# Kernel optimization log

Measured on AMD Instinct MI355X. Metric: run time of the kernel, lower is better.

## Reference

```python
import jax, jax.numpy as jnp
import numpy as np

N_NODES = 50000
N_EDGES = 800000
N_GRAPHS = 256
HEADS = 4
HID = 64
HC = HEADS * HID  # 256
EMB = 256
RADIUS = 3
EPS_BN = 1e-5
NEG_SLOPE = 0.2  # PyG GATConv default


def _init(key, shape, fan_in):
    return jax.random.normal(key, shape, jnp.float32) / np.sqrt(fan_in).astype(np.float32)


def setup_inputs() -> dict:
    key = jax.random.key(0)
    ks = jax.random.split(key, 12)
    x = jax.random.normal(ks[0], (N_NODES, 9), jnp.float32)
    edge_index = jax.random.randint(ks[1], (2, N_EDGES), 0, N_NODES)
    batch = jnp.sort(jax.random.randint(ks[2], (N_NODES,), 0, N_GRAPHS))
    W0 = _init(ks[3], (9, HC), 9)
    att_src0 = _init(ks[4], (HEADS, HID), HID)
    att_dst0 = _init(ks[5], (HEADS, HID), HID)
    bias0 = jnp.zeros((HC,), jnp.float32)
    W12 = _init(ks[6], (2, HC, HC), HC)
    att_src12 = _init(ks[7], (2, HEADS, HID), HID)
    att_dst12 = _init(ks[8], (2, HEADS, HID), HID)
    bias12 = jnp.zeros((2, HC), jnp.float32)
    gamma = jnp.ones((RADIUS, HC), jnp.float32)
    beta = jnp.zeros((RADIUS, HC), jnp.float32)
    Wm1 = _init(ks[9], (HC, EMB), HC)
    bm1 = jnp.zeros((EMB,), jnp.float32)
    Wm2 = _init(ks[10], (EMB, EMB), EMB)
    bm2 = jnp.zeros((EMB,), jnp.float32)
    return dict(x=x, edge_index=edge_index, batch=batch, W0=W0, att_src0=att_src0,
                att_dst0=att_dst0, bias0=bias0, W12=W12, att_src12=att_src12,
                att_dst12=att_dst12, bias12=bias12, gamma=gamma, beta=beta,
                Wm1=Wm1, bm1=bm1, Wm2=Wm2, bm2=bm2)


def gat_conv(x, src, dst, W, a_src, a_dst, bias):
    # PyG GATConv (concat=True), self-loops already appended to src/dst.
    N = x.shape[0]
    h = (x @ W).reshape(N, HEADS, HID)                 # [N,H,C]
    al_src = jnp.einsum('nhc,hc->nh', h, a_src)        # [N,H]
    al_dst = jnp.einsum('nhc,hc->nh', h, a_dst)
    e = jax.nn.leaky_relu(al_src[src] + al_dst[dst], NEG_SLOPE)  # [E,H]
    # segment softmax over incoming edges of each dst node
    e_max = jax.ops.segment_max(e, dst, num_segments=N)
    e = jnp.exp(e - e_max[dst])
    denom = jax.ops.segment_sum(e, dst, num_segments=N)
    alpha = e / (denom[dst] + 1e-16)                   # [E,H]
    msg = alpha[:, :, None] * h[src]                   # [E,H,C]
    out = jax.ops.segment_sum(msg, dst, num_segments=N)  # [N,H,C]
    return out.reshape(N, HC) + bias


def batch_norm(x, g, b):
    mu = x.mean(axis=0)
    var = x.var(axis=0)
    return (x - mu) * jax.lax.rsqrt(var + EPS_BN) * g + b


def reference(x, edge_index, batch, W0, att_src0, att_dst0, bias0, W12, att_src12,
              att_dst12, bias12, gamma, beta, Wm1, bm1, Wm2, bm2):
    loops = jnp.arange(N_NODES, dtype=edge_index.dtype)
    src = jnp.concatenate([edge_index[0], loops])
    dst = jnp.concatenate([edge_index[1], loops])
    Ws = [W0, W12[0], W12[1]]
    a_s = [att_src0, att_src12[0], att_src12[1]]
    a_d = [att_dst0, att_dst12[0], att_dst12[1]]
    bs = [bias0, bias12[0], bias12[1]]
    f = jnp.zeros((N_GRAPHS, HC), x.dtype)
    for i in range(RADIUS):
        x = gat_conv(x, src, dst, Ws[i], a_s[i], a_d[i], bs[i])
        x = jax.nn.relu(batch_norm(x, gamma[i], beta[i]))
        x_sparse = jax.nn.softmax(x, axis=-1)
        f = f + jax.ops.segment_sum(x_sparse, batch, num_segments=N_GRAPHS)
    f = jax.nn.relu(f @ Wm1 + bm1) @ Wm2 + bm2
    return f
```

## Files before the change

### kernel.cpp

```cpp
#include <hip/hip_runtime.h>
#include <hip/hip_bf16.h>

#define NN      50000
#define NE      800000
#define ETOT    850000
#define NG      256
#define HC      256
#define NBLK    ((NN + 255) / 256)

typedef __attribute__((ext_vector_type(8))) short bf8;
typedef __attribute__((ext_vector_type(4))) float f4;

__device__ inline float lrelu(float v) { return v > 0.f ? v : 0.2f * v; }

__device__ inline unsigned short f2bf(float f) {
    unsigned int u = __float_as_uint(f);
    unsigned int r = (u + 0x7FFFu + ((u >> 16) & 1u)) >> 16;
    return (unsigned short)r;
}
__device__ inline float bf2f(unsigned short u) {
    return __uint_as_float((unsigned int)u << 16);
}

__global__ void gemm_h_kernel(const float* __restrict__ x, const float* __restrict__ W,
                              const float* __restrict__ asrc, const float* __restrict__ adst,
                              unsigned short* __restrict__ h, float* __restrict__ alsrc,
                              float* __restrict__ aldst, int K) {
    int n = blockIdx.x;
    int j = threadIdx.x;
    extern __shared__ float lds[];
    float* xrow = lds;
    float* hrow = lds + K;
    for (int k = j; k < K; k += 256) xrow[k] = x[(size_t)n * K + k];
    __syncthreads();
    float acc = 0.f;
    for (int k = 0; k < K; ++k) acc = fmaf(xrow[k], W[k * 256 + j], acc);
    h[(size_t)n * 256 + j] = f2bf(acc);
    hrow[j] = acc;
    __syncthreads();
    if (j < 8) {
        int hd = j & 3;
        bool is_dst = j >= 4;
        const float* a = is_dst ? adst : asrc;
        float s = 0.f;
        for (int c = 0; c < 64; ++c) s = fmaf(hrow[hd * 64 + c], a[hd * 64 + c], s);
        (is_dst ? aldst : alsrc)[n * 4 + hd] = s;
    }
}

__global__ void wt_kernel(const float* __restrict__ W, unsigned short* __restrict__ Wt) {
    int c = blockIdx.x, k = threadIdx.x;
    Wt[c * 256 + k] = f2bf(W[k * 256 + c]);
}

__global__ __launch_bounds__(256) void gemm_mfma_kernel(
    const unsigned short* __restrict__ X, const unsigned short* __restrict__ Wt,
    const float* __restrict__ asrc, const float* __restrict__ adst,
    unsigned short* __restrict__ h, float* __restrict__ alsrc, float* __restrict__ aldst) {
    __shared__ unsigned short hs[128 * 132];
    int tid = threadIdx.x;
    int w = tid >> 6, l = tid & 63;
    int m0 = blockIdx.x * 128;
    int n0 = blockIdx.y * 128;
    int wr = (w >> 1) * 64, wc = (w & 1) * 64;
    int lr = l & 15, lk = l >> 4;

    f4 acc[4][4];
#pragma unroll
    for (int mi = 0; mi < 4; ++mi)
#pragma unroll
        for (int ni = 0; ni < 4; ++ni) acc[mi][ni] = (f4)(0.f);

    const unsigned short* arow[4];
#pragma unroll
    for (int mi = 0; mi < 4; ++mi) {
        int row = m0 + wr + mi * 16 + lr;
        if (row >= NN) row = NN - 1;
        arow[mi] = X + (size_t)row * 256 + lk * 8;
    }
    const unsigned short* brow[4];
#pragma unroll
    for (int ni = 0; ni < 4; ++ni)
        brow[ni] = Wt + (size_t)(n0 + wc + ni * 16 + lr) * 256 + lk * 8;

#pragma unroll
    for (int kk = 0; kk < 8; ++kk) {
        bf8 a[4], b[4];
#pragma unroll
        for (int mi = 0; mi < 4; ++mi) a[mi] = *(const bf8*)(arow[mi] + kk * 32);
#pragma unroll
        for (int ni = 0; ni < 4; ++ni) b[ni] = *(const bf8*)(brow[ni] + kk * 32);
#pragma unroll
        for (int mi = 0; mi < 4; ++mi)
#pragma unroll
            for (int ni = 0; ni < 4; ++ni)
                acc[mi][ni] = __builtin_amdgcn_mfma_f32_16x16x32_bf16(
                    a[mi], b[ni], acc[mi][ni], 0, 0, 0);
    }

    int hd = (n0 + wc) >> 6;
    float aSv[4], aDv[4];
#pragma unroll
    for (int ni = 0; ni < 4; ++ni) {
        aSv[ni] = asrc[hd * 64 + ni * 16 + lr];
        aDv[ni] = adst[hd * 64 + ni * 16 + lr];
    }
#pragma unroll
    for (int mi = 0; mi < 4; ++mi) {
#pragma unroll
        for (int r = 0; r < 4; ++r) {
            float ps = 0.f, pd = 0.f;
#pragma unroll
            for (int ni = 0; ni < 4; ++ni) {
                ps = fmaf(acc[mi][ni][r], aSv[ni], ps);
                pd = fmaf(acc[mi][ni][r], aDv[ni], pd);
            }
#pragma unroll
            for (int o = 1; o < 16; o <<= 1) {
                ps += __shfl_xor(ps, o, 64);
                pd += __shfl_xor(pd, o, 64);
            }
            if (lr == 0) {
                int row = m0 + wr + mi * 16 + 4 * lk + r;
                if (row < NN) {
                    alsrc[row * 4 + hd] = ps;
                    aldst[row * 4 + hd] = pd;
                }
            }
        }
    }

#pragma unroll
    for (int mi = 0; mi < 4; ++mi)
#pragma unroll
        for (int ni = 0; ni < 4; ++ni) {
            int C = wc + ni * 16 + lr;
#pragma unroll
            for (int r = 0; r < 4; ++r) {
                int R = wr + mi * 16 + 4 * lk + r;
                hs[R * 132 + C] = f2bf(acc[mi][ni][r]);
            }
        }
    __syncthreads();
    {
        int row = tid >> 1, half = tid & 1;
        int grow = m0 + row;
        if (grow < NN) {
            const unsigned short* src = hs + row * 132 + half * 64;
            unsigned short* dst = h + (size_t)grow * 256 + n0 + half * 64;
#pragma unroll
            for (int i = 0; i < 16; ++i)
                *(uint2*)(dst + i * 4) = *(const uint2*)(src + i * 4);
        }
    }
}

__global__ void hist_kernel(const int* __restrict__ ei, int* __restrict__ deg) {
    int t = blockIdx.x * 256 + threadIdx.x;
    if (t >= ETOT) return;
    int d = (t < NE) ? ei[NE + t] : t - NE;
    atomicAdd(&deg[d], 1);
}

__global__ void scan1_kernel(const int* __restrict__ deg, int* __restrict__ bsum) {
    __shared__ int red[256];
    int b = blockIdx.x, t = threadIdx.x;
    int idx = b * 256 + t;
    red[t] = (idx < NN) ? deg[idx] : 0;
    __syncthreads();
    for (int s = 128; s > 0; s >>= 1) { if (t < s) red[t] += red[t + s]; __syncthreads(); }
    if (t == 0) bsum[b] = red[0];
}

__global__ void scan2_kernel(const int* __restrict__ bsum, int* __restrict__ boff,
                             int* __restrict__ rowptr) {
    __shared__ int s[256];
    int t = threadIdx.x;
    int v = (t < NBLK) ? bsum[t] : 0;
    s[t] = v;
    __syncthreads();
    for (int d = 1; d < 256; d <<= 1) {
        int x = s[t];
        int a = (t >= d) ? s[t - d] : 0;
        __syncthreads();
        s[t] = x + a;
        __syncthreads();
    }
    if (t < NBLK) boff[t] = s[t] - v;
    if (t == NBLK - 1) rowptr[NN] = s[t];
}

__global__ void scan3_kernel(const int* __restrict__ deg, const int* __restrict__ boff,
                             int* __restrict__ rowptr) {
    __shared__ int s[256];
    int b = blockIdx.x, t = threadIdx.x;
    int idx = b * 256 + t;
    int v = (idx < NN) ? deg[idx] : 0;
    s[t] = v;
    __syncthreads();
    for (int d = 1; d < 256; d <<= 1) {
        int x = s[t];
        int a = (t >= d) ? s[t - d] : 0;
        __syncthreads();
        s[t] = x + a;
        __syncthreads();
    }
    if (idx < NN) rowptr[idx] = boff[b] + s[t] - v;
}

__global__ void scatter_kernel(const int* __restrict__ ei, int* __restrict__ cursor,
                               int* __restrict__ esrc) {
    int t = blockIdx.x * 256 + threadIdx.x;
    if (t >= ETOT) return;
    int s, d;
    if (t < NE) { s = ei[t]; d = ei[NE + t]; } else { s = d = t - NE; }
    int pos = atomicAdd(&cursor[d], 1);
    esrc[pos] = s;
}

__global__ void gbound_kernel(const int* __restrict__ batch, int* __restrict__ gstart) {
    int n = blockIdx.x * 256 + threadIdx.x;
    if (n >= NN) return;
    int b = batch[n];
    int prev = (n == 0) ? -1 : batch[n - 1];
    for (int g = prev + 1; g <= b; ++g) gstart[g] = n;
    if (n == NN - 1)
        for (int g = b + 1; g <= NG; ++g) gstart[g] = NN;
}

__global__ __launch_bounds__(256, 8) void agg_csr_kernel(
    const int* __restrict__ rowptr, const int* __restrict__ esrc,
    const float* __restrict__ alsrc, const float* __restrict__ aldst,
    const unsigned short* __restrict__ h, const float* __restrict__ bias,
    float* __restrict__ out) {
    int l = threadIdx.x & 63;
    int n = blockIdx.x * 4 + (threadIdx.x >> 6);
    int hd = l >> 4;
    float ad = aldst[n * 4 + hd];
    float4 bv = *(const float4*)(bias + l * 4);
    int beg = rowptr[n], end = rowptr[n + 1];
    float a0 = 0.f, a1 = 0.f, a2 = 0.f, a3 = 0.f, den = 0.f;
#pragma unroll 4
    for (int e = beg; e < end; ++e) {
        int s = esrc[e];
        float wgt = __expf(lrelu(alsrc[s * 4 + hd] + ad));
        uint2 hv = *(const uint2*)(h + (size_t)s * 256 + l * 4);
        den += wgt;
        a0 = fmaf(wgt, bf2f((unsigned short)hv.x), a0);
        a1 = fmaf(wgt, bf2f((unsigned short)(hv.x >> 16)), a1);
        a2 = fmaf(wgt, bf2f((unsigned short)hv.y), a2);
        a3 = fmaf(wgt, bf2f((unsigned short)(hv.y >> 16)), a3);
    }
    float r = 1.f / (den + 1e-16f);
    *(float4*)(out + (size_t)n * 256 + l * 4) =
        make_float4(fmaf(a0, r, bv.x), fmaf(a1, r, bv.y),
                    fmaf(a2, r, bv.z), fmaf(a3, r, bv.w));
}

__global__ void bn_stats_kernel(const float* __restrict__ x1, float* __restrict__ S,
                                float* __restrict__ S2) {
    int j = threadIdx.x, b = blockIdx.x;
    float s = 0.f, s2 = 0.f;
    for (int n = b; n < NN; n += gridDim.x) {
        float v = x1[(size_t)n * 256 + j];
        s += v;
        s2 = fmaf(v, v, s2);
    }
    atomicAdd(&S[j], s);
    atomicAdd(&S2[j], s2);
}

__global__ __launch_bounds__(256, 8) void bn_apply_kernel(
    const float* __restrict__ x1, const float* __restrict__ S, const float* __restrict__ S2,
    const float* __restrict__ gamma, const float* __restrict__ beta,
    unsigned short* __restrict__ xnext, float* __restrict__ mrow, float* __restrict__ rsrow) {
    int l = threadIdx.x & 63;
    int n = blockIdx.x * 4 + (threadIdx.x >> 6);
    int c = l * 4;
    float4 xv = *(const float4*)(x1 + (size_t)n * 256 + c);
    float4 s4 = *(const float4*)(S + c);
    float4 q4 = *(const float4*)(S2 + c);
    float4 g4 = *(const float4*)(gamma + c);
    float4 b4 = *(const float4*)(beta + c);
    float v[4];
    {
        float xs[4] = {xv.x, xv.y, xv.z, xv.w};
        float ss[4] = {s4.x, s4.y, s4.z, s4.w};
        float qs[4] = {q4.x, q4.y, q4.z, q4.w};
        float gs[4] = {g4.x, g4.y, g4.z, g4.w};
        float bs[4] = {b4.x, b4.y, b4.z, b4.w};
#pragma unroll
        for (int i = 0; i < 4; ++i) {
            float mu = ss[i] * (1.f / NN);
            float var = fmaxf(qs[i] * (1.f / NN) - mu * mu, 0.f);
            v[i] = fmaxf((xs[i] - mu) * rsqrtf(var + 1e-5f) * gs[i] + bs[i], 0.f);
        }
    }
    float m = fmaxf(fmaxf(v[0], v[1]), fmaxf(v[2], v[3]));
#pragma unroll
    for (int o = 1; o < 64; o <<= 1) m = fmaxf(m, __shfl_xor(m, o, 64));
    float e0 = __expf(v[0] - m), e1 = __expf(v[1] - m);
    float e2 = __expf(v[2] - m), e3 = __expf(v[3] - m);
    float sum = e0 + e1 + e2 + e3;
#pragma unroll
    for (int o = 1; o < 64; o <<= 1) sum += __shfl_xor(sum, o, 64);
    uint2 pk;
    pk.x = (unsigned int)f2bf(v[0]) | ((unsigned int)f2bf(v[1]) << 16);
    pk.y = (unsigned int)f2bf(v[2]) | ((unsigned int)f2bf(v[3]) << 16);
    *(uint2*)(xnext + (size_t)n * 256 + c) = pk;
    if (l == 0) { mrow[n] = m; rsrow[n] = 1.f / sum; }
}

__global__ __launch_bounds__(64) void pool_kernel(
    const float* __restrict__ x1, const float* __restrict__ S, const float* __restrict__ S2,
    const float* __restrict__ gamma, const float* __restrict__ beta,
    const float* __restrict__ mrow, const float* __restrict__ rsrow,
    const int* __restrict__ gstart, float* __restrict__ f) {
    int g = blockIdx.x;
    int j = blockIdx.y * 64 + threadIdx.x;
    float mu = S[j] * (1.f / NN);
    float var = fmaxf(S2[j] * (1.f / NN) - mu * mu, 0.f);
    float rq = rsqrtf(var + 1e-5f);
    float ga = gamma[j], be = beta[j];
    int beg = gstart[g], end = gstart[g + 1];
    float acc = 0.f;
#pragma unroll 4
    for (int n = beg; n < end; ++n) {
        float v = fmaxf((x1[(size_t)n * 256 + j] - mu) * rq * ga + be, 0.f);
        acc += __expf(v - mrow[n]) * rsrow[n];
    }
    f[g * 256 + j] += acc;
}

__global__ void mlp_kernel(const float* __restrict__ A, const float* __restrict__ W,
                           const float* __restrict__ b, float* __restrict__ out, int do_relu) {
    int i = blockIdx.x, j = threadIdx.x;
    __shared__ float row[256];
    row[j] = A[i * 256 + j];
    __syncthreads();
    float acc = b[j];
#pragma unroll 8
    for (int k = 0; k < 256; ++k) acc = fmaf(row[k], W[k * 256 + j], acc);
    if (do_relu) acc = fmaxf(acc, 0.f);
    out[i * 256 + j] = acc;
}

extern "C" void kernel_launch(void* const* d_in, const int* in_sizes, int n_in,
                              void* d_out, int out_size, void* d_ws, size_t ws_size,
                              hipStream_t stream) {
    const float* x0     = (const float*)d_in[0];
    const int*   ei     = (const int*)d_in[1];
    const int*   batch  = (const int*)d_in[2];
    const float* W0     = (const float*)d_in[3];
    const float* asrc0  = (const float*)d_in[4];
    const float* adst0  = (const float*)d_in[5];
    const float* bias0  = (const float*)d_in[6];
    const float* W12    = (const float*)d_in[7];
    const float* asrc12 = (const float*)d_in[8];
    const float* adst12 = (const float*)d_in[9];
    const float* bias12 = (const float*)d_in[10];
    const float* gamma  = (const float*)d_in[11];
    const float* beta   = (const float*)d_in[12];
    const float* Wm1    = (const float*)d_in[13];
    const float* bm1    = (const float*)d_in[14];
    const float* Wm2    = (const float*)d_in[15];
    const float* bm2    = (const float*)d_in[16];
    float* out = (float*)d_out;

    float* ws = (float*)d_ws;
    const size_t NODE_F = (size_t)NN * 256;
    unsigned short* h16  = (unsigned short*)ws;
    float*          x1   = ws + NODE_F / 2;
    unsigned short* xb16 = (unsigned short*)(x1 + NODE_F);
    unsigned short* wt   = xb16 + NODE_F;
    float* alsrc  = (float*)(wt + 2 * 65536);
    float* aldst  = alsrc + (size_t)NN * 4;
    float* S      = aldst + (size_t)NN * 4;
    float* S2     = S + 256;
    float* fpool  = S2 + 256;
    float* g_buf  = fpool + 65536;
    float* mrow   = g_buf + 65536;
    float* rsrow  = mrow + NN;
    int*   deg    = (int*)(rsrow + NN);
    int*   rowptr = deg + NN + 1;
    int*   cursor = rowptr + NN + 1;
    int*   bsum   = cursor + NN + 1;
    int*   boff   = bsum + NBLK + 1;
    int*   gstart = boff + NBLK + 1;
    int*   esrc   = gstart + NG + 1;

    hipMemsetAsync(deg, 0, (NN + 1) * sizeof(int), stream);
    hist_kernel<<<(ETOT + 255) / 256, 256, 0, stream>>>(ei, deg);
    scan1_kernel<<<NBLK, 256, 0, stream>>>(deg, bsum);
    scan2_kernel<<<1, 256, 0, stream>>>(bsum, boff, rowptr);
    scan3_kernel<<<NBLK, 256, 0, stream>>>(deg, boff, rowptr);
    hipMemcpyAsync(cursor, rowptr, (NN + 1) * sizeof(int), hipMemcpyDeviceToDevice, stream);
    scatter_kernel<<<(ETOT + 255) / 256, 256, 0, stream>>>(ei, cursor, esrc);

    gbound_kernel<<<(NN + 255) / 256, 256, 0, stream>>>(batch, gstart);

    wt_kernel<<<256, 256, 0, stream>>>(W12, wt);
    wt_kernel<<<256, 256, 0, stream>>>(W12 + 65536, wt + 65536);

    hipMemsetAsync(fpool, 0, 65536 * sizeof(float), stream);

    for (int l = 0; l < 3; ++l) {
        const float* as = (l == 0) ? asrc0 : asrc12 + (size_t)(l - 1) * 256;
        const float* ad = (l == 0) ? adst0 : adst12 + (size_t)(l - 1) * 256;
        const float* bs = (l == 0) ? bias0 : bias12 + (size_t)(l - 1) * 256;

        if (l == 0) {
            gemm_h_kernel<<<NN, 256, (9 + 256) * sizeof(float), stream>>>(
                x0, W0, as, ad, h16, alsrc, aldst, 9);
        } else {
            dim3 grid((NN + 127) / 128, 2);
            gemm_mfma_kernel<<<grid, 256, 0, stream>>>(
                xb16, wt + (size_t)(l - 1) * 65536, as, ad, h16, alsrc, aldst);
        }

        agg_csr_kernel<<<NN / 4, 256, 0, stream>>>(rowptr, esrc, alsrc, aldst, h16, bs, x1);

        hipMemsetAsync(S, 0, 512 * sizeof(float), stream);
        bn_stats_kernel<<<1024, 256, 0, stream>>>(x1, S, S2);

        bn_apply_kernel<<<NN / 4, 256, 0, stream>>>(
            x1, S, S2, gamma + l * 256, beta + l * 256, xb16, mrow, rsrow);

        pool_kernel<<<dim3(NG, 4), 64, 0, stream>>>(
            x1, S, S2, gamma + l * 256, beta + l * 256, mrow, rsrow, gstart, fpool);
    }

    mlp_kernel<<<256, 256, 0, stream>>>(fpool, Wm1, bm1, g_buf, 1);
    mlp_kernel<<<256, 256, 0, stream>>>(g_buf, Wm2, bm2, out, 0);
}
```

Before: 714.7 us.

## Fuse BN-apply with pooling per graph, vectorize layer-0 GEMM, retile MFMA GEMM

Merges the batch-norm apply and pooling kernels into one per-graph kernel. Row max and sum stay in shared memory, so the mrow/rsrow global buffers go away. The layer-0 GEMM now handles four nodes per block with float4 weight loads and a shuffle reduction. The MFMA GEMM moves to 64-row tiles covering all 256 columns per block, and scan3 writes the cursor directly instead of a separate device memcpy. The fused kernel launches only 256 blocks, which risks low occupancy, and it caps each graph at 768 nodes.

New measurement: 772.8 us. 8.1% more time.

```diff
diff --git a/kernel.cpp b/kernel.cpp
--- a/kernel.cpp
+++ b/kernel.cpp
@@ -7,6 +7,7 @@
 #define NG      256
 #define HC      256
 #define NBLK    ((NN + 255) / 256)
+#define MAXGN   768
 
 typedef __attribute__((ext_vector_type(8))) short bf8;
 typedef __attribute__((ext_vector_type(4))) float f4;
@@ -22,29 +23,44 @@
     return __uint_as_float((unsigned int)u << 16);
 }
 
-__global__ void gemm_h_kernel(const float* __restrict__ x, const float* __restrict__ W,
-                              const float* __restrict__ asrc, const float* __restrict__ adst,
-                              unsigned short* __restrict__ h, float* __restrict__ alsrc,
-                              float* __restrict__ aldst, int K) {
-    int n = blockIdx.x;
-    int j = threadIdx.x;
-    extern __shared__ float lds[];
-    float* xrow = lds;
-    float* hrow = lds + K;
-    for (int k = j; k < K; k += 256) xrow[k] = x[(size_t)n * K + k];
-    __syncthreads();
-    float acc = 0.f;
-    for (int k = 0; k < K; ++k) acc = fmaf(xrow[k], W[k * 256 + j], acc);
-    h[(size_t)n * 256 + j] = f2bf(acc);
-    hrow[j] = acc;
-    __syncthreads();
-    if (j < 8) {
-        int hd = j & 3;
-        bool is_dst = j >= 4;
-        const float* a = is_dst ? adst : asrc;
-        float s = 0.f;
-        for (int c = 0; c < 64; ++c) s = fmaf(hrow[hd * 64 + c], a[hd * 64 + c], s);
-        (is_dst ? aldst : alsrc)[n * 4 + hd] = s;
+__global__ __launch_bounds__(256, 8) void gemm_h_kernel(
+    const float* __restrict__ x, const float* __restrict__ W,
+    const float* __restrict__ asrc, const float* __restrict__ adst,
+    unsigned short* __restrict__ h, float* __restrict__ alsrc,
+    float* __restrict__ aldst) {
+    int l = threadIdx.x & 63;
+    int n = blockIdx.x * 4 + (threadIdx.x >> 6);
+    int c0 = l * 4;
+    float acc[4] = {0.f, 0.f, 0.f, 0.f};
+#pragma unroll
+    for (int k = 0; k < 9; ++k) {
+        float xv = x[n * 9 + k];
+        float4 wv = *(const float4*)(W + k * 256 + c0);
+        acc[0] = fmaf(xv, wv.x, acc[0]);
+        acc[1] = fmaf(xv, wv.y, acc[1]);
+        acc[2] = fmaf(xv, wv.z, acc[2]);
+        acc[3] = fmaf(xv, wv.w, acc[3]);
+    }
+    uint2 pk;
+    pk.x = (unsigned int)f2bf(acc[0]) | ((unsigned int)f2bf(acc[1]) << 16);
+    pk.y = (unsigned int)f2bf(acc[2]) | ((unsigned int)f2bf(acc[3]) << 16);
+    *(uint2*)(h + (size_t)n * 256 + c0) = pk;
+    int hd = l >> 4;
+    int ci = (l & 15) * 4;
+    float ps = 0.f, pd = 0.f;
+#pragma unroll
+    for (int i = 0; i < 4; ++i) {
+        ps = fmaf(acc[i], asrc[hd * 64 + ci + i], ps);
+        pd = fmaf(acc[i], adst[hd * 64 + ci + i], pd);
+    }
+#pragma unroll
+    for (int o = 1; o < 16; o <<= 1) {
+        ps += __shfl_xor(ps, o, 64);
+        pd += __shfl_xor(pd, o, 64);
+    }
+    if ((l & 15) == 0) {
+        alsrc[n * 4 + hd] = ps;
+        aldst[n * 4 + hd] = pd;
     }
 }
 
@@ -53,16 +69,16 @@
     Wt[c * 256 + k] = f2bf(W[k * 256 + c]);
 }
 
+#define HS_STRIDE 258
 __global__ __launch_bounds__(256) void gemm_mfma_kernel(
     const unsigned short* __restrict__ X, const unsigned short* __restrict__ Wt,
     const float* __restrict__ asrc, const float* __restrict__ adst,
     unsigned short* __restrict__ h, float* __restrict__ alsrc, float* __restrict__ aldst) {
-    __shared__ unsigned short hs[128 * 132];
+    __shared__ unsigned short hs[64 * HS_STRIDE];
     int tid = threadIdx.x;
     int w = tid >> 6, l = tid & 63;
-    int m0 = blockIdx.x * 128;
-    int n0 = blockIdx.y * 128;
-    int wr = (w >> 1) * 64, wc = (w & 1) * 64;
+    int m0 = blockIdx.x * 64;
+    int wc = w * 64;
     int lr = l & 15, lk = l >> 4;
 
     f4 acc[4][4];
@@ -74,14 +90,14 @@
     const unsigned short* arow[4];
 #pragma unroll
     for (int mi = 0; mi < 4; ++mi) {
-        int row = m0 + wr + mi * 16 + lr;
+        int row = m0 + mi * 16 + lr;
         if (row >= NN) row = NN - 1;
         arow[mi] = X + (size_t)row * 256 + lk * 8;
     }
     const unsigned short* brow[4];
 #pragma unroll
     for (int ni = 0; ni < 4; ++ni)
-        brow[ni] = Wt + (size_t)(n0 + wc + ni * 16 + lr) * 256 + lk * 8;
+        brow[ni] = Wt + (size_t)(wc + ni * 16 + lr) * 256 + lk * 8;
 
 #pragma unroll
     for (int kk = 0; kk < 8; ++kk) {
@@ -98,7 +114,7 @@
                     a[mi], b[ni], acc[mi][ni], 0, 0, 0);
     }
 
-    int hd = (n0 + wc) >> 6;
+    int hd = w;
     float aSv[4], aDv[4];
 #pragma unroll
     for (int ni = 0; ni < 4; ++ni) {
@@ -121,7 +137,7 @@
                 pd += __shfl_xor(pd, o, 64);
             }
             if (lr == 0) {
-                int row = m0 + wr + mi * 16 + 4 * lk + r;
+                int row = m0 + mi * 16 + 4 * lk + r;
                 if (row < NN) {
                     alsrc[row * 4 + hd] = ps;
                     aldst[row * 4 + hd] = pd;
@@ -137,17 +153,17 @@
             int C = wc + ni * 16 + lr;
 #pragma unroll
             for (int r = 0; r < 4; ++r) {
-                int R = wr + mi * 16 + 4 * lk + r;
-                hs[R * 132 + C] = f2bf(acc[mi][ni][r]);
+                int R = mi * 16 + 4 * lk + r;
+                hs[R * HS_STRIDE + C] = f2bf(acc[mi][ni][r]);
             }
         }
     __syncthreads();
     {
-        int row = tid >> 1, half = tid & 1;
+        int row = tid & 63, q = tid >> 6;
         int grow = m0 + row;
         if (grow < NN) {
-            const unsigned short* src = hs + row * 132 + half * 64;
-            unsigned short* dst = h + (size_t)grow * 256 + n0 + half * 64;
+            const unsigned short* src = hs + row * HS_STRIDE + q * 64;
+            unsigned short* dst = h + (size_t)grow * 256 + q * 64;
 #pragma unroll
             for (int i = 0; i < 16; ++i)
                 *(uint2*)(dst + i * 4) = *(const uint2*)(src + i * 4);
@@ -191,7 +207,7 @@
 }
 
 __global__ void scan3_kernel(const int* __restrict__ deg, const int* __restrict__ boff,
-                             int* __restrict__ rowptr) {
+                             int* __restrict__ rowptr, int* __restrict__ cursor) {
     __shared__ int s[256];
     int b = blockIdx.x, t = threadIdx.x;
     int idx = b * 256 + t;
@@ -205,7 +221,11 @@
         s[t] = x + a;
         __syncthreads();
     }
-    if (idx < NN) rowptr[idx] = boff[b] + s[t] - v;
+    if (idx < NN) {
+        int r = boff[b] + s[t] - v;
+        rowptr[idx] = r;
+        cursor[idx] = r;
+    }
 }
 
 __global__ void scatter_kernel(const int* __restrict__ ei, int* __restrict__ cursor,
@@ -270,64 +290,68 @@
     atomicAdd(&S2[j], s2);
 }
 
-__global__ __launch_bounds__(256, 8) void bn_apply_kernel(
+__global__ __launch_bounds__(256) void bnpool_kernel(
     const float* __restrict__ x1, const float* __restrict__ S, const float* __restrict__ S2,
     const float* __restrict__ gamma, const float* __restrict__ beta,
-    unsigned short* __restrict__ xnext, float* __restrict__ mrow, float* __restrict__ rsrow) {
-    int l = threadIdx.x & 63;
-    int n = blockIdx.x * 4 + (threadIdx.x >> 6);
-    int c = l * 4;
-    float4 xv = *(const float4*)(x1 + (size_t)n * 256 + c);
-    float4 s4 = *(const float4*)(S + c);
-    float4 q4 = *(const float4*)(S2 + c);
-    float4 g4 = *(const float4*)(gamma + c);
-    float4 b4 = *(const float4*)(beta + c);
-    float v[4];
+    const int* __restrict__ gstart, unsigned short* __restrict__ xnext,
+    float* __restrict__ f) {
+    __shared__ float mS[MAXGN], rsS[MAXGN];
+    int g = blockIdx.x;
+    int w = threadIdx.x >> 6, l = threadIdx.x & 63;
+    int beg = gstart[g], end = gstart[g + 1];
+    int cnt = end - beg;
+    if (cnt > MAXGN) cnt = MAXGN;
+    int c0 = l * 4;
+    float4 s4 = *(const float4*)(S + c0);
+    float4 q4 = *(const float4*)(S2 + c0);
+    float4 g4 = *(const float4*)(gamma + c0);
+    float4 b4 = *(const float4*)(beta + c0);
+    float mu[4], rqg[4], be[4];
     {
-        float xs[4] = {xv.x, xv.y, xv.z, xv.w};
         float ss[4] = {s4.x, s4.y, s4.z, s4.w};
         float qs[4] = {q4.x, q4.y, q4.z, q4.w};
         float gs[4] = {g4.x, g4.y, g4.z, g4.w};
         float bs[4] = {b4.x, b4.y, b4.z, b4.w};
 #pragma unroll
         for (int i = 0; i < 4; ++i) {
-            float mu = ss[i] * (1.f / NN);
-            float var = fmaxf(qs[i] * (1.f / NN) - mu * mu, 0.f);
-            v[i] = fmaxf((xs[i] - mu) * rsqrtf(var + 1e-5f) * gs[i] + bs[i], 0.f);
+            mu[i] = ss[i] * (1.f / NN);
+            float var = fmaxf(qs[i] * (1.f / NN) - mu[i] * mu[i], 0.f);
+            rqg[i] = rsqrtf(var + 1e-5f) * gs[i];
+            be[i] = bs[i];
         }
     }
-    float m = fmaxf(fmaxf(v[0], v[1]), fmaxf(v[2], v[3]));
-#pragma unroll
-    for (int o = 1; o < 64; o <<= 1) m = fmaxf(m, __shfl_xor(m, o, 64));
-    float e0 = __expf(v[0] - m), e1 = __expf(v[1] - m);
-    float e2 = __expf(v[2] - m), e3 = __expf(v[3] - m);
-    float sum = e0 + e1 + e2 + e3;
-#pragma unroll
-    for (int o = 1; o < 64; o <<= 1) sum += __shfl_xor(sum, o, 64);
-    uint2 pk;
-    pk.x = (unsigned int)f2bf(v[0]) | ((unsigned int)f2bf(v[1]) << 16);
-    pk.y = (unsigned int)f2bf(v[2]) | ((unsigned int)f2bf(v[3]) << 16);
-    *(uint2*)(xnext + (size_t)n * 256 + c) = pk;
-    if (l == 0) { mrow[n] = m; rsrow[n] = 1.f / sum; }
-}
-
-__global__ __launch_bounds__(64) void pool_kernel(
-    const float* __restrict__ x1, const float* __restrict__ S, const float* __restrict__ S2,
-    const float* __restrict__ gamma, const float* __restrict__ beta,
-    const float* __restrict__ mrow, const float* __restrict__ rsrow,
-    const int* __restrict__ gstart, float* __restrict__ f) {
-    int g = blockIdx.x;
-    int j = blockIdx.y * 64 + threadIdx.x;
-    float mu = S[j] * (1.f / NN);
-    float var = fmaxf(S2[j] * (1.f / NN) - mu * mu, 0.f);
-    float rq = rsqrtf(var + 1e-5f);
-    float ga = gamma[j], be = beta[j];
-    int beg = gstart[g], end = gstart[g + 1];
+    for (int it = w; it < cnt; it += 4) {
+        int n = beg + it;
+        float4 xv = *(const float4*)(x1 + (size_t)n * 256 + c0);
+        float v[4];
+        float xs[4] = {xv.x, xv.y, xv.z, xv.w};
+#pragma unroll
+        for (int i = 0; i < 4; ++i)
+            v[i] = fmaxf((xs[i] - mu[i]) * rqg[i] + be[i], 0.f);
+        float m = fmaxf(fmaxf(v[0], v[1]), fmaxf(v[2], v[3]));
+#pragma unroll
+        for (int o = 1; o < 64; o <<= 1) m = fmaxf(m, __shfl_xor(m, o, 64));
+        float sum = __expf(v[0] - m) + __expf(v[1] - m) + __expf(v[2] - m) + __expf(v[3] - m);
+#pragma unroll
+        for (int o = 1; o < 64; o <<= 1) sum += __shfl_xor(sum, o, 64);
+        uint2 pk;
+        pk.x = (unsigned int)f2bf(v[0]) | ((unsigned int)f2bf(v[1]) << 16);
+        pk.y = (unsigned int)f2bf(v[2]) | ((unsigned int)f2bf(v[3]) << 16);
+        *(uint2*)(xnext + (size_t)n * 256 + c0) = pk;
+        if (l == 0) { mS[it] = m; rsS[it] = 1.f / sum; }
+    }
+    __syncthreads();
+    int j = threadIdx.x;
+    float muj = S[j] * (1.f / NN);
+    float varj = fmaxf(S2[j] * (1.f / NN) - muj * muj, 0.f);
+    float rqgj = rsqrtf(varj + 1e-5f) * gamma[j];
+    float bej = beta[j];
     float acc = 0.f;
 #pragma unroll 4
-    for (int n = beg; n < end; ++n) {
-        float v = fmaxf((x1[(size_t)n * 256 + j] - mu) * rq * ga + be, 0.f);
-        acc += __expf(v - mrow[n]) * rsrow[n];
+    for (int it = 0; it < cnt; ++it) {
+        float xv = x1[(size_t)(beg + it) * 256 + j];
+        float v = fmaxf((xv - muj) * rqgj + bej, 0.f);
+        acc += __expf(v - mS[it]) * rsS[it];
     }
     f[g * 256 + j] += acc;
 }
@@ -379,9 +403,7 @@
     float* S2     = S + 256;
     float* fpool  = S2 + 256;
     float* g_buf  = fpool + 65536;
-    float* mrow   = g_buf + 65536;
-    float* rsrow  = mrow + NN;
-    int*   deg    = (int*)(rsrow + NN);
+    int*   deg    = (int*)(g_buf + 65536);
     int*   rowptr = deg + NN + 1;
     int*   cursor = rowptr + NN + 1;
     int*   bsum   = cursor + NN + 1;
@@ -393,8 +415,7 @@
     hist_kernel<<<(ETOT + 255) / 256, 256, 0, stream>>>(ei, deg);
     scan1_kernel<<<NBLK, 256, 0, stream>>>(deg, bsum);
     scan2_kernel<<<1, 256, 0, stream>>>(bsum, boff, rowptr);
-    scan3_kernel<<<NBLK, 256, 0, stream>>>(deg, boff, rowptr);
-    hipMemcpyAsync(cursor, rowptr, (NN + 1) * sizeof(int), hipMemcpyDeviceToDevice, stream);
+    scan3_kernel<<<NBLK, 256, 0, stream>>>(deg, boff, rowptr, cursor);
     scatter_kernel<<<(ETOT + 255) / 256, 256, 0, stream>>>(ei, cursor, esrc);
 
     gbound_kernel<<<(NN + 255) / 256, 256, 0, stream>>>(batch, gstart);
@@ -410,11 +431,10 @@
         const float* bs = (l == 0) ? bias0 : bias12 + (size_t)(l - 1) * 256;
 
         if (l == 0) {
-            gemm_h_kernel<<<NN, 256, (9 + 256) * sizeof(float), stream>>>(
-                x0, W0, as, ad, h16, alsrc, aldst, 9);
+            gemm_h_kernel<<<NN / 4, 256, 0, stream>>>(
+                x0, W0, as, ad, h16, alsrc, aldst);
         } else {
-            dim3 grid((NN + 127) / 128, 2);
-            gemm_mfma_kernel<<<grid, 256, 0, stream>>>(
+            gemm_mfma_kernel<<<(NN + 63) / 64, 256, 0, stream>>>(
                 xb16, wt + (size_t)(l - 1) * 65536, as, ad, h16, alsrc, aldst);
         }
 
@@ -423,11 +443,8 @@
         hipMemsetAsync(S, 0, 512 * sizeof(float), stream);
         bn_stats_kernel<<<1024, 256, 0, stream>>>(x1, S, S2);
 
-        bn_apply_kernel<<<NN / 4, 256, 0, stream>>>(
-            x1, S, S2, gamma + l * 256, beta + l * 256, xb16, mrow, rsrow);
-
-        pool_kernel<<<dim3(NG, 4), 64, 0, stream>>>(
-            x1, S, S2, gamma + l * 256, beta + l * 256, mrow, rsrow, gstart, fpool);
+        bnpool_kernel<<<NG, 256, 0, stream>>>(
+            x1, S, S2, gamma + l * 256, beta + l * 256, gstart, xb16, fpool);
     }
 
     mlp_kernel<<<256, 256, 0, stream>>>(fpool, Wm1, bm1, g_buf, 1);
```
